# Performance work log

Hardware: AMD Instinct MI355X
Metric: run time of the kernel (lower is better)

Reference implementation:

```python
import jax, jax.numpy as jnp
import numpy as np

ROUTING_ITER = 2
EPS = 1e-8


def squash(s, axis):
    # s * ||s||^2 / (1 + ||s||^2) / ||s||
    sq = jnp.sum(s * s, axis=axis, keepdims=True)
    return s * (sq / (1.0 + sq)) / jnp.sqrt(sq + EPS)


def setup_inputs() -> dict:
    key = jax.random.key(0)
    k1, k2 = jax.random.split(key)
    B, N_in, d_in = 64, 2048, 16
    J, D = 32, 16  # num_capsule, dim_capsule
    x = jax.random.normal(k1, (B, N_in, 1, d_in), dtype=jnp.float32)
    weight = jax.random.normal(k2, (1, N_in, J, D, d_in), dtype=jnp.float32) * 0.05
    return {"x": x, "weight": weight}


def reference(x, weight):
    # x: [B, N_in, 1, d_in]; weight: [1, N_in, J, D, d_in]
    # prediction vectors u[b,i,j,:] = W[i,j] @ x[b,i]
    u = jnp.einsum('ijde,bie->bijd', weight[0], x[:, :, 0, :])  # [B,N_in,J,D]
    B, N_in, J, D = u.shape

    # dynamic routing on stop_gradient(u)
    u_sg = jax.lax.stop_gradient(u)
    b = jnp.zeros((B, N_in, J, 1), dtype=u.dtype)
    for _ in range(ROUTING_ITER):
        c = jax.nn.softmax(b, axis=2)                      # [B,N_in,J,1]
        s = jnp.sum(u_sg * c, axis=1, keepdims=True)       # [B,1,J,D]
        v = squash(s, axis=2)                              # squash over capsule axis (faithful)
        b = b + jnp.sum(u_sg * v, axis=-1, keepdims=True)  # [B,N_in,J,1]

    c = jax.nn.softmax(b, axis=2)
    s = jnp.sum(u * c, axis=1)  # [B,J,D]
    return squash(s, axis=-1)
```

## Files before the change

kernel.cpp:

```cpp
#include <hip/hip_runtime.h>

typedef __attribute__((ext_vector_type(8))) short short8;
typedef __attribute__((ext_vector_type(4))) float f32x4;
typedef __attribute__((ext_vector_type(2))) float f32x2;
typedef __attribute__((ext_vector_type(4))) unsigned int uint4v;
typedef unsigned short u16;
typedef unsigned long long u64;

#define NI 2048

__device__ __forceinline__ unsigned int packbf2(float a, float b){
  unsigned int ua = __float_as_uint(a), ub = __float_as_uint(b);
  unsigned int ra = (ua + 0x7FFFu + ((ua >> 16) & 1u)) >> 16;
  unsigned int rb = (ub + 0x7FFFu + ((ub >> 16) & 1u)) & 0xFFFF0000u;
  return ra | rb;
}
__device__ __forceinline__ float bflo(unsigned int p){ return __uint_as_float(p << 16); }
__device__ __forceinline__ float bfhi(unsigned int p){ return __uint_as_float(p & 0xFFFF0000u); }

__device__ __forceinline__ uint4v cvt8(const f32x4& a, const f32x4& b){
  uint4v p = { packbf2(a.x, a.y), packbf2(a.z, a.w),
               packbf2(b.x, b.y), packbf2(b.z, b.w) };
  return p;
}

__device__ __forceinline__ void gl_lds16(const void* g, void* l){
  __builtin_amdgcn_global_load_lds(
      (const __attribute__((address_space(1))) unsigned int*)g,
      (__attribute__((address_space(3))) unsigned int*)l, 16, 0, 0);
}

union F2U { f32x2 f; u64 u; };

__device__ __forceinline__ void st_u64_coh(float* p, float a, float b){
  F2U v; v.f.x = a; v.f.y = b;
  __hip_atomic_store((u64*)p, v.u, __ATOMIC_RELAXED, __HIP_MEMORY_SCOPE_AGENT);
}
__device__ __forceinline__ f32x2 ld_f2_coh(const float* p){
  F2U v; v.u = __hip_atomic_load((const u64*)p, __ATOMIC_RELAXED, __HIP_MEMORY_SCOPE_AGENT);
  return v.f;
}
__device__ __forceinline__ f32x4 ld_f4_coh(const float* p){
  f32x2 a = ld_f2_coh(p), b = ld_f2_coh(p + 2);
  f32x4 r; r.x = a.x; r.y = a.y; r.z = b.x; r.w = b.y; return r;
}
__device__ __forceinline__ void st_f4_coh(float* p, const f32x4& v){
  st_u64_coh(p, v.x, v.y); st_u64_coh(p + 2, v.z, v.w);
}
__device__ __forceinline__ float ld_f_coh(const float* p){
  return __hip_atomic_load((const float*)p, __ATOMIC_RELAXED, __HIP_MEMORY_SCOPE_AGENT);
}


#define FUSED_SMEM 152576

template<int MODE>
__device__ __forceinline__ void pass_phase(
    const u16* __restrict__ sW, const u16* __restrict__ sX,
    float* __restrict__ sSumA, float* __restrict__ sSumB,
    const float* __restrict__ Sv1, const float* __restrict__ qv1,
    const float* __restrict__ Sv2, const float* __restrict__ qv2,
    float* __restrict__ partials, int blk, int t)
{
  const int w = t >> 6, lane = t & 63;
  const int wtile = w & 1, jhalf = (w >> 1) & 1, bh = w >> 2;
  const int lq = lane >> 4, lb = lane & 15, qs = lq & 1;
  const int bg = bh * 32 + wtile * 16 + lb;
  const short8 zero8 = {0,0,0,0,0,0,0,0};
  const f32x4 zf4 = {0.f,0.f,0.f,0.f};

  f32x4 acc[16];
  #pragma unroll
  for (int tj = 0; tj < 16; ++tj) acc[tj] = zf4;

  unsigned int vpl[16], vph[16];
  if constexpr (MODE >= 1){
    f32x4 qa = ld_f4_coh(qv1 + bg * 16 + lq * 4);
    f32x4 fa;
    fa.x = qa.x / ((1.f + qa.x) * sqrtf(qa.x + 1e-8f));
    fa.y = qa.y / ((1.f + qa.y) * sqrtf(qa.y + 1e-8f));
    fa.z = qa.z / ((1.f + qa.z) * sqrtf(qa.z + 1e-8f));
    fa.w = qa.w / ((1.f + qa.w) * sqrtf(qa.w + 1e-8f));
    f32x4 fb = zf4;
    if constexpr (MODE == 2){
      f32x4 qb = ld_f4_coh(qv2 + bg * 16 + lq * 4);
      fb.x = qb.x / ((1.f + qb.x) * sqrtf(qb.x + 1e-8f));
      fb.y = qb.y / ((1.f + qb.y) * sqrtf(qb.y + 1e-8f));
      fb.z = qb.z / ((1.f + qb.z) * sqrtf(qb.z + 1e-8f));
      fb.w = qb.w / ((1.f + qb.w) * sqrtf(qb.w + 1e-8f));
    }
    #pragma unroll
    for (int tj = 0; tj < 16; ++tj){
      int jd = (jhalf * 16 + tj) * 16 + lq * 4;
      f32x4 sv = ld_f4_coh(Sv1 + bg * 512 + jd);
      f32x4 v;
      v.x = sv.x * fa.x; v.y = sv.y * fa.y; v.z = sv.z * fa.z; v.w = sv.w * fa.w;
      if constexpr (MODE == 2){
        f32x4 s2 = ld_f4_coh(Sv2 + bg * 512 + jd);
        v.x += s2.x * fb.x; v.y += s2.y * fb.y; v.z += s2.z * fb.z; v.w += s2.w * fb.w;
      }
      vpl[tj] = packbf2(v.x, v.y);
      vph[tj] = packbf2(v.z, v.w);
    }
  }

  if constexpr (MODE == 0){
    const int rsel = lq >> 1;
    #pragma unroll
    for (int s = 0; s < 4; ++s){
      const u16* wrow = sW + (size_t)(2 * s + rsel) * 8192;
      const u16* xrow = sX + (size_t)(2 * s + rsel) * 1024;
      short8 bfrag = *(const short8*)(xrow + bg * 16 + qs * 8);
      #pragma unroll
      for (int tj = 0; tj < 16; ++tj){
        int j = jhalf * 16 + tj;
        short8 afrag = *(const short8*)(wrow + j * 256 + lb * 16 + qs * 8);
        acc[tj] = __builtin_amdgcn_mfma_f32_16x16x32_bf16(afrag, bfrag, acc[tj], 0, 0, 0);
      }
    }
  } else {
    for (int s = 0; s < 8; ++s){
      const u16* wrow = sW + (size_t)s * 8192;
      const u16* xrow = sX + (size_t)s * 1024;
      short8 bl8 = *(const short8*)(xrow + bg * 16 + qs * 8);
      short8 bfrag = (lq < 2) ? bl8 : zero8;
      f32x4 ut[16];
      float e[16];
      float ps = 0.f;
      #pragma unroll
      for (int tj = 0; tj < 16; ++tj){
        int j = jhalf * 16 + tj;
        short8 afrag = *(const short8*)(wrow + j * 256 + lb * 16 + qs * 8);
        ut[tj] = __builtin_amdgcn_mfma_f32_16x16x32_bf16(afrag, bfrag, zf4, 0, 0, 0);
        float p = ut[tj].x * bflo(vpl[tj]) + ut[tj].y * bfhi(vpl[tj])
                + ut[tj].z * bflo(vph[tj]) + ut[tj].w * bfhi(vph[tj]);
        p += __shfl_xor(p, 16, 64);
        p += __shfl_xor(p, 32, 64);
        e[tj] = __expf(p);
        ps += e[tj];
      }
      float* sS = (s & 1) ? sSumB : sSumA;
      if (lane < 16) sS[w * 16 + lane] = ps;
      __syncthreads();
      float inv = 1.0f / (ps + sS[(w ^ 2) * 16 + lb]);
      #pragma unroll
      for (int tj = 0; tj < 16; ++tj){
        float c = e[tj] * inv;
        acc[tj].x += c * ut[tj].x;
        acc[tj].y += c * ut[tj].y;
        acc[tj].z += c * ut[tj].z;
        acc[tj].w += c * ut[tj].w;
      }
    }
  }

  float* dst = partials + ((size_t)blk * 8 + (size_t)w) * 4096 + (size_t)lane * 64;
  #pragma unroll
  for (int tj = 0; tj < 16; ++tj) st_f4_coh(dst + tj * 4, acc[tj]);
}

__device__ __forceinline__ void reduce_phase(
    const float* __restrict__ partials, float* __restrict__ S,
    float* __restrict__ qbd, float* __restrict__ qbj,
    float scale, float* __restrict__ sRed, int blk, int t)
{
  const int pr = t & 63;
  const int dg = t >> 6;
  const int o  = blk * 128 + pr * 2;
  const float* src = partials + (size_t)dg * 32 * 32768 + (size_t)o;
  float a0 = 0.f, a1 = 0.f;
  #pragma unroll 8
  for (int p = 0; p < 32; ++p){
    f32x2 v = ld_f2_coh(src + (size_t)p * 32768);
    a0 += v.x; a1 += v.y;
  }
  sRed[t * 2]     = a0;
  sRed[t * 2 + 1] = a1;
  __syncthreads();
  if (t < 64){
    float t0 = 0.f, t1 = 0.f;
    #pragma unroll
    for (int g = 0; g < 8; ++g){
      t0 += sRed[(g * 64 + t) * 2];
      t1 += sRed[(g * 64 + t) * 2 + 1];
    }
    t0 *= scale; t1 *= scale;
    const int oo = blk * 128 + t * 2;
    const int bh = oo >> 14, wd = (oo >> 12) & 3, ln = (oo >> 6) & 63, k = oo & 63;
    const int b = bh * 32 + (wd & 1) * 16 + (ln & 15);
    const int j = (wd >> 1) * 16 + (k >> 2);
    const int d = ((ln >> 4) << 2) + (k & 3);
    st_u64_coh(S + b * 512 + j * 16 + d, t0, t1);
    if (qbd){
      atomicAdd(qbd + b * 16 + d,     t0 * t0);
      atomicAdd(qbd + b * 16 + d + 1, t1 * t1);
    }
    if (qbj){
      atomicAdd(qbj + b * 32 + j, t0 * t0 + t1 * t1);
    }
  }
  __syncthreads();
}

__global__ __launch_bounds__(512, 2)
void caps_fused(const float* __restrict__ X, const float* __restrict__ W,
                unsigned int* __restrict__ gcnt,
                float* __restrict__ qb1, float* __restrict__ qb2,
                float* __restrict__ qb3,
                float* __restrict__ S1, float* __restrict__ S2, float* __restrict__ S3,
                float* __restrict__ partials, float* __restrict__ out)
{
  extern __shared__ __align__(16) char smem[];
  u16* sW = (u16*)smem;
  u16* sX = (u16*)(smem + 131072);
  float* sSumA = (float*)(smem + 147456);
  float* sSumB = sSumA + 128;
  float* sRed  = sSumB + 128;

  const int t = threadIdx.x;
  const int blk = blockIdx.x;
  const size_t i0 = (size_t)blk * 8;

  {
    const float* wsrc = W + i0 * 8192;
    #pragma unroll
    for (int k = 0; k < 16; ++k){
      int idx = k * 4096 + t * 8;
      f32x4 a = *(const f32x4*)(wsrc + idx);
      f32x4 b = *(const f32x4*)(wsrc + idx + 4);
      *(uint4v*)(sW + idx) = cvt8(a, b);
    }
    int r = t >> 6, b = t & 63;
    const float* xs = X + ((size_t)b * NI + i0 + (size_t)r) * 16;
    f32x4 a0 = *(const f32x4*)(xs);
    f32x4 a1 = *(const f32x4*)(xs + 4);
    f32x4 a2 = *(const f32x4*)(xs + 8);
    f32x4 a3 = *(const f32x4*)(xs + 12);
    *(uint4v*)(sX + t * 16)     = cvt8(a0, a1);
    *(uint4v*)(sX + t * 16 + 8) = cvt8(a2, a3);
  }
  __syncthreads();

  unsigned int gen = 0;
  auto gridsync = [&](){
    ++gen;
    __syncthreads();
    if (t == 0){
      __hip_atomic_fetch_add(gcnt, 1u, __ATOMIC_RELAXED, __HIP_MEMORY_SCOPE_AGENT);
      const unsigned int target = gen * 256u;
      while (__hip_atomic_load(gcnt, __ATOMIC_RELAXED, __HIP_MEMORY_SCOPE_AGENT) < target)
        __builtin_amdgcn_s_sleep(8);
    }
    __syncthreads();
  };

  pass_phase<0>(sW, sX, sSumA, sSumB, nullptr, nullptr, nullptr, nullptr, partials, blk, t);
  gridsync();
  reduce_phase(partials, S1, qb1, nullptr, 1.0f / 32.0f, sRed, blk, t);
  gridsync();

  pass_phase<1>(sW, sX, sSumA, sSumB, S1, qb1, nullptr, nullptr, partials, blk, t);
  gridsync();
  reduce_phase(partials, S2, qb2, nullptr, 1.0f, sRed, blk, t);
  gridsync();

  pass_phase<2>(sW, sX, sSumA, sSumB, S1, qb1, S2, qb2, partials, blk, t);
  gridsync();
  reduce_phase(partials, S3, nullptr, qb3, 1.0f, sRed, blk, t);
  gridsync();

  if (blk < 64){
    float s = ld_f_coh(S3 + blk * 512 + t);
    float q = ld_f_coh(qb3 + blk * 32 + (t >> 4));
    out[blk * 512 + t] = s * (q / ((1.f + q) * sqrtf(q + 1e-8f)));
  }
}


__global__ __launch_bounds__(256)
void caps_prep(const float* __restrict__ W, const float* __restrict__ X,
               u16* __restrict__ Wb, u16* __restrict__ Xb)
{
  const int bid = blockIdx.x;
  if (bid < 8192){
    size_t base = (size_t)bid * 2048 + (size_t)threadIdx.x * 8;
    f32x4 a = *(const f32x4*)(W + base);
    f32x4 b = *(const f32x4*)(W + base + 4);
    *(uint4v*)(Wb + base) = cvt8(a, b);
  } else {
    int p = (bid - 8192) * 256 + threadIdx.x;
    int i = p >> 6, b = p & 63;
    const float* src = X + ((size_t)b * NI + i) * 16;
    f32x4 a0 = *(const f32x4*)(src);
    f32x4 a1 = *(const f32x4*)(src + 4);
    f32x4 a2 = *(const f32x4*)(src + 8);
    f32x4 a3 = *(const f32x4*)(src + 12);
    *(uint4v*)(Xb + (size_t)p * 16)     = cvt8(a0, a1);
    *(uint4v*)(Xb + (size_t)p * 16 + 8) = cvt8(a2, a3);
  }
}

template<int MODE>
__global__ __launch_bounds__(256, 2)
void caps_pass_f(const u16* __restrict__ Wb,
                 const u16* __restrict__ Xb,
                 const float* __restrict__ vbuf,
                 float* __restrict__ partials, int CI)
{
  constexpr int WR = (MODE == 0) ? 2 : 1;
  __shared__ __align__(16) u16 sW[2][WR * 8192];
  __shared__ __align__(16) u16 sX[2][WR * 512];
  __shared__ float sSum[4][16];

  const int t     = threadIdx.x;
  const int w     = t >> 6;
  const int lane  = t & 63;
  const int wtile = w & 1;
  const int jhalf = w >> 1;
  const int lq    = lane >> 4;
  const int lb    = lane & 15;
  const int q1    = lq & 1;
  const int bhalf = blockIdx.x & 1;
  const int iblk  = blockIdx.x >> 1;
  const int bloc  = wtile * 16 + lb;
  const int bg    = bhalf * 32 + bloc;
  const size_t i0 = (size_t)iblk * (size_t)CI;

  const short8 zero8 = {0,0,0,0,0,0,0,0};
  const f32x4  zf4   = {0.f,0.f,0.f,0.f};

  f32x4 acc[16];
  #pragma unroll
  for (int tj = 0; tj < 16; ++tj) acc[tj] = zf4;

  unsigned int vpl[16], vph[16];
  if constexpr (MODE == 1){
    #pragma unroll
    for (int tj = 0; tj < 16; ++tj){
      f32x4 v = *(const f32x4*)(&vbuf[bg * 512 + (jhalf * 16 + tj) * 16 + lq * 4]);
      vpl[tj] = packbf2(v.x, v.y);
      vph[tj] = packbf2(v.z, v.w);
    }
  }

  auto stage = [&](int nb, size_t irow){
    #pragma unroll
    for (int rr = 0; rr < WR; ++rr){
      const u16* src = Wb + (irow + rr) * 8192 + (size_t)(w * 4) * 512;
      u16* dst = &sW[nb][rr * 8192 + w * 4 * 512];
      #pragma unroll
      for (int r = 0; r < 4; ++r)
        gl_lds16(src + r * 512 + lane * 8, dst + r * 512);
    }
    if (w >= 4 - WR){
      int rr = w - (4 - WR);
      gl_lds16(Xb + ((irow + rr) * 64 + (size_t)bhalf * 32) * 16 + lane * 8,
               &sX[nb][rr * 512]);
    }
  };

  const int NSTEP = CI / WR;
  stage(0, i0);
  __syncthreads();

  for (int s = 0; s < NSTEP; ++s){
    const int buf = s & 1;
    if (s + 1 < NSTEP) stage(buf ^ 1, i0 + (size_t)(s + 1) * WR);

    if constexpr (MODE == 0){
      const int rsel = lq >> 1;
      short8 bfrag = *(const short8*)(&sX[buf][rsel * 512 + bloc * 16 + q1 * 8]);
      #pragma unroll
      for (int tj = 0; tj < 16; ++tj){
        int j = jhalf * 16 + tj;
        short8 afrag = *(const short8*)(&sW[buf][rsel * 8192 + j * 256 + lb * 16 + q1 * 8]);
        acc[tj] = __builtin_amdgcn_mfma_f32_16x16x32_bf16(afrag, bfrag, acc[tj], 0, 0, 0);
      }
    } else {
      short8 bl8 = *(const short8*)(&sX[buf][bloc * 16 + q1 * 8]);
      short8 bfrag = (lq < 2) ? bl8 : zero8;
      f32x4 ut[16];
      float e[16];
      float ps = 0.f;
      #pragma unroll
      for (int tj = 0; tj < 16; ++tj){
        int j = jhalf * 16 + tj;
        short8 al8 = *(const short8*)(&sW[buf][j * 256 + lb * 16 + q1 * 8]);
        short8 afrag = (lq < 2) ? al8 : zero8;
        ut[tj] = __builtin_amdgcn_mfma_f32_16x16x32_bf16(afrag, bfrag, zf4, 0, 0, 0);
        float p = ut[tj].x * bflo(vpl[tj]) + ut[tj].y * bfhi(vpl[tj])
                + ut[tj].z * bflo(vph[tj]) + ut[tj].w * bfhi(vph[tj]);
        p += __shfl_xor(p, 16, 64);
        p += __shfl_xor(p, 32, 64);
        e[tj] = __expf(p);
        ps += e[tj];
      }
      if (lane < 16) sSum[w][lane] = ps;
      __syncthreads();
      float inv = 1.0f / (ps + sSum[w ^ 2][lb]);
      #pragma unroll
      for (int tj = 0; tj < 16; ++tj){
        float c = e[tj] * inv;
        acc[tj].x += c * ut[tj].x;
        acc[tj].y += c * ut[tj].y;
        acc[tj].z += c * ut[tj].z;
        acc[tj].w += c * ut[tj].w;
      }
    }
    __syncthreads();
  }

  float* dst = partials + ((size_t)blockIdx.x * 4 + (size_t)w) * 4096 + (size_t)lane * 64;
  #pragma unroll
  for (int tj = 0; tj < 16; ++tj) *(f32x4*)(dst + tj * 4) = acc[tj];
}

template<int MODE>
__global__ __launch_bounds__(256)
void caps_pass_legacy(const float* __restrict__ Wg, const float* __restrict__ Xg,
                      const float* __restrict__ vbuf, float* __restrict__ partials, int CI)
{
  __shared__ __align__(16) unsigned short sW[2][8192];
  __shared__ __align__(16) unsigned int   sXd[2][256];
  __shared__ float sLog[(MODE == 1) ? (32 * 33) : 4];
  const int t = threadIdx.x, w = t >> 6, lane = t & 63;
  const int wtile = w & 1, jhalf = w >> 1, lq = lane >> 4, lb = lane & 15, q1 = lq & 1;
  const int bhalf = blockIdx.x & 1, iblk = blockIdx.x >> 1;
  const int bloc = wtile * 16 + lb, bg = bhalf * 32 + bloc;
  const size_t i0 = (size_t)iblk * (size_t)CI;
  const short8 zero8 = {0,0,0,0,0,0,0,0};
  const f32x4 zf4 = {0.f,0.f,0.f,0.f};
  f32x4 acc[16];
  #pragma unroll
  for (int tj = 0; tj < 16; ++tj) acc[tj] = zf4;
  unsigned int vpl[16], vph[16];
  if constexpr (MODE == 1){
    #pragma unroll
    for (int tj = 0; tj < 16; ++tj){
      f32x4 v = *(const f32x4*)(&vbuf[bg * 512 + (jhalf * 16 + tj) * 16 + lq * 4]);
      vpl[tj] = packbf2(v.x, v.y); vph[tj] = packbf2(v.z, v.w);
    }
  }
  {
    const float* wsrc = Wg + i0 * 8192;
    #pragma unroll
    for (int r = 0; r < 4; ++r){
      int c = r * 256 + t;
      f32x4 a = *(const f32x4*)(&wsrc[c * 8]);
      f32x4 b = *(const f32x4*)(&wsrc[c * 8 + 4]);
      *(uint4v*)(&sW[0][c * 8]) = cvt8(a, b);
    }
    int bidx = bhalf * 32 + (t >> 3), e2 = t & 7;
    f32x2 xv = *(const f32x2*)(&Xg[((size_t)bidx * NI + i0) * 16 + e2 * 2]);
    sXd[0][t] = packbf2(xv.x, xv.y);
  }
  __syncthreads();
  for (int s = 0; s < CI; ++s){
    const int buf = s & 1;
    f32x4 wpa[4], wpb[4]; f32x2 xp;
    const bool more = (s + 1 < CI);
    if (more){
      const float* wsrc = Wg + (i0 + (size_t)(s + 1)) * 8192;
      #pragma unroll
      for (int r = 0; r < 4; ++r){
        int c = r * 256 + t;
        wpa[r] = *(const f32x4*)(&wsrc[c * 8]);
        wpb[r] = *(const f32x4*)(&wsrc[c * 8 + 4]);
      }
      int bidx = bhalf * 32 + (t >> 3), e2 = t & 7;
      xp = *(const f32x2*)(&Xg[((size_t)bidx * NI + i0 + s + 1) * 16 + e2 * 2]);
    }
    const unsigned short* xrow = (const unsigned short*)&sXd[buf][0];
    short8 bl8 = *(const short8*)(&xrow[bloc * 16 + q1 * 8]);
    short8 bfrag = (lq < 2) ? bl8 : zero8;
    if constexpr (MODE == 0){
      #pragma unroll
      for (int tj = 0; tj < 16; ++tj){
        int j = jhalf * 16 + tj;
        short8 al8 = *(const short8*)(&sW[buf][j * 256 + lb * 16 + q1 * 8]);
        short8 afrag = (lq < 2) ? al8 : zero8;
        acc[tj] = __builtin_amdgcn_mfma_f32_16x16x32_bf16(afrag, bfrag, acc[tj], 0, 0, 0);
      }
    } else {
      #pragma unroll
      for (int tj = 0; tj < 16; ++tj){
        int j = jhalf * 16 + tj;
        short8 al8 = *(const short8*)(&sW[buf][j * 256 + lb * 16 + q1 * 8]);
        short8 afrag = (lq < 2) ? al8 : zero8;
        f32x4 u = __builtin_amdgcn_mfma_f32_16x16x32_bf16(afrag, bfrag, zf4, 0, 0, 0);
        float p = u.x * bflo(vpl[tj]) + u.y * bfhi(vpl[tj])
                + u.z * bflo(vph[tj]) + u.w * bfhi(vph[tj]);
        p += __shfl_xor(p, 16, 64);
        p += __shfl_xor(p, 32, 64);
        if (lane < 16) sLog[bloc * 33 + j] = p;
      }
      __syncthreads();
      const float* logrow = &sLog[bloc * 33];
      float ssum = 0.f;
      #pragma unroll
      for (int jj = 0; jj < 32; ++jj) ssum += __expf(logrow[jj]);
      float inv = 1.0f / ssum;
      #pragma unroll
      for (int tj = 0; tj < 16; ++tj){
        int j = jhalf * 16 + tj;
        short8 al8 = *(const short8*)(&sW[buf][j * 256 + lb * 16 + q1 * 8]);
        short8 afrag = (lq < 2) ? al8 : zero8;
        f32x4 u = __builtin_amdgcn_mfma_f32_16x16x32_bf16(afrag, bfrag, zf4, 0, 0, 0);
        float c = __expf(logrow[j]) * inv;
        acc[tj].x += c * u.x; acc[tj].y += c * u.y;
        acc[tj].z += c * u.z; acc[tj].w += c * u.w;
      }
    }
    if (more){
      const int nb = buf ^ 1;
      #pragma unroll
      for (int r = 0; r < 4; ++r){
        int c = r * 256 + t;
        *(uint4v*)(&sW[nb][c * 8]) = cvt8(wpa[r], wpb[r]);
      }
      sXd[nb][t] = packbf2(xp.x, xp.y);
    }
    __syncthreads();
  }
  float* dst = partials + ((size_t)blockIdx.x * 4 + (size_t)w) * 4096 + (size_t)lane * 64;
  #pragma unroll
  for (int tj = 0; tj < 16; ++tj) *(f32x4*)(dst + tj * 4) = acc[tj];
}

template<int NBLK>
__global__ __launch_bounds__(128)
void caps_reduce(const float* __restrict__ partials, float* __restrict__ S_buf, float scale)
{
  const int T = blockIdx.x * 128 + threadIdx.x;
  float s0 = 0.f, s1 = 0.f, s2 = 0.f, s3 = 0.f;
  #pragma unroll
  for (int bl = 0; bl < NBLK; bl += 4){
    s0 += partials[(size_t)(bl + 0) * 32768 + T];
    s1 += partials[(size_t)(bl + 1) * 32768 + T];
    s2 += partials[(size_t)(bl + 2) * 32768 + T];
    s3 += partials[(size_t)(bl + 3) * 32768 + T];
  }
  float s = ((s0 + s1) + (s2 + s3)) * scale;
  const int bhalf = T >> 14, w = (T >> 12) & 3, l = (T >> 6) & 63, k = T & 63;
  const int b  = bhalf * 32 + (w & 1) * 16 + (l & 15);
  const int jd = ((w >> 1) * 16 + (k >> 2)) * 16 + ((l >> 4) << 2) + (k & 3);
  S_buf[b * 512 + jd] = s;
}

__global__ __launch_bounds__(256)
void caps_squash_j(const float* __restrict__ S, const float* __restrict__ vprev,
                   float* __restrict__ vout)
{
  const int b = blockIdx.x, t = threadIdx.x;
  __shared__ float sq[16];
  if (t < 16) sq[t] = 0.f;
  __syncthreads();
  float s0 = S[b * 512 + t], s1 = S[b * 512 + 256 + t];
  atomicAdd(&sq[t & 15], s0 * s0 + s1 * s1);
  __syncthreads();
  float q = sq[t & 15];
  float f = q / ((1.f + q) * sqrtf(q + 1e-8f));
  float v0 = s0 * f, v1 = s1 * f;
  if (vprev){ v0 += vprev[b * 512 + t]; v1 += vprev[b * 512 + 256 + t]; }
  vout[b * 512 + t] = v0;
  vout[b * 512 + 256 + t] = v1;
}

__global__ __launch_bounds__(256)
void caps_squash_d(const float* __restrict__ S, float* __restrict__ out)
{
  const int b = blockIdx.x, t = threadIdx.x;
  __shared__ float sq[32];
  if (t < 32) sq[t] = 0.f;
  __syncthreads();
  float s0 = S[b * 512 + t], s1 = S[b * 512 + 256 + t];
  atomicAdd(&sq[t >> 4], s0 * s0);
  atomicAdd(&sq[(t + 256) >> 4], s1 * s1);
  __syncthreads();
  float q0 = sq[t >> 4], q1 = sq[(t + 256) >> 4];
  out[b * 512 + t]       = s0 * q0 / ((1.f + q0) * sqrtf(q0 + 1e-8f));
  out[b * 512 + 256 + t] = s1 * q1 / ((1.f + q1) * sqrtf(q1 + 1e-8f));
}

extern "C" void kernel_launch(void* const* d_in, const int* in_sizes, int n_in,
                              void* d_out, int out_size, void* d_ws, size_t ws_size,
                              hipStream_t stream)
{
  const float* X = (const float*)d_in[0];
  const float* W = (const float*)d_in[1];
  float* wsf = (float*)d_ws;

  const size_t OF_Q1   = 64;
  const size_t OF_Q2   = OF_Q1 + 1024;
  const size_t OF_Q3   = OF_Q2 + 1024;
  const size_t OF_S1   = OF_Q3 + 2048;
  const size_t OF_S2   = OF_S1 + 32768;
  const size_t OF_S3   = OF_S2 + 32768;
  const size_t OF_PART = OF_S3 + 32768;
  const size_t FUSED_FLOATS = OF_PART + (size_t)256 * 32768;

  static int fused_ok = -1;
  if (fused_ok < 0){
    fused_ok = 0;
    hipFuncSetAttribute(reinterpret_cast<const void*>(caps_fused),
                        hipFuncAttributeMaxDynamicSharedMemorySize, FUSED_SMEM);
    int dev = 0, ncu = 0, nb = 0;
    hipGetDevice(&dev);
    hipDeviceGetAttribute(&ncu, hipDeviceAttributeMultiprocessorCount, dev);
    hipError_t e = hipOccupancyMaxActiveBlocksPerMultiprocessor(
        &nb, caps_fused, 512, (size_t)FUSED_SMEM);
    if (e == hipSuccess && nb >= 1 && ncu >= 256) fused_ok = 1;
  }

  if (fused_ok == 1 && ws_size >= FUSED_FLOATS * 4){
    hipMemsetAsync(d_ws, 0, (64 + 1024 + 1024 + 2048) * 4, stream);
    caps_fused<<<dim3(256), dim3(512), FUSED_SMEM, stream>>>(
        X, W, (unsigned int*)wsf,
        wsf + OF_Q1, wsf + OF_Q2, wsf + OF_Q3,
        wsf + OF_S1, wsf + OF_S2, wsf + OF_S3, wsf + OF_PART, (float*)d_out);
    return;
  }

  const size_t FP = (size_t)256 * 32768;
  const size_t WB_ELE = (size_t)NI * 8192, XB_ELE = (size_t)NI * 64 * 16;
  const size_t need_full = (FP + 3 * 32768) * 4 + (WB_ELE + XB_ELE) * 2;

  if (ws_size >= need_full){
    float* partials = wsf;
    float* sbuf = wsf + FP;
    float* v1   = sbuf + 32768;
    float* v12  = v1 + 32768;
    u16* Wb = (u16*)(v12 + 32768);
    u16* Xb = Wb + WB_ELE;

    caps_prep<<<dim3(8704), dim3(256), 0, stream>>>(W, X, Wb, Xb);

    caps_pass_f<0><<<dim3(512), dim3(256), 0, stream>>>(Wb, Xb, nullptr, partials, 8);
    caps_reduce<256><<<dim3(256), dim3(128), 0, stream>>>(partials, sbuf, 1.0f / 32.0f);
    caps_squash_j<<<dim3(64), dim3(256), 0, stream>>>(sbuf, nullptr, v1);

    caps_pass_f<1><<<dim3(512), dim3(256), 0, stream>>>(Wb, Xb, v1, partials, 8);
    caps_reduce<256><<<dim3(256), dim3(128), 0, stream>>>(partials, sbuf, 1.0f);
    caps_squash_j<<<dim3(64), dim3(256), 0, stream>>>(sbuf, v1, v12);

    caps_pass_f<1><<<dim3(512), dim3(256), 0, stream>>>(Wb, Xb, v12, partials, 8);
    caps_reduce<256><<<dim3(256), dim3(128), 0, stream>>>(partials, sbuf, 1.0f);
    caps_squash_d<<<dim3(64), dim3(256), 0, stream>>>(sbuf, (float*)d_out);
  } else {
    int NBI = 256;
    auto need = [](int nb){ return ((size_t)nb * 32768 + 3 * 32768) * 4; };
    if (ws_size < need(256)){
      if      (ws_size >= need(64)) NBI = 64;
      else if (ws_size >= need(16)) NBI = 16;
      else                          NBI = 4;
    }
    const int CI = NI / NBI;
    float* partials = wsf;
    float* sbuf = wsf + (size_t)NBI * 32768;
    float* v1   = sbuf + 32768;
    float* v12  = v1 + 32768;
    auto reduce = [&](float scale){
      if      (NBI == 256) caps_reduce<256><<<dim3(256), dim3(128), 0, stream>>>(partials, sbuf, scale);
      else if (NBI ==  64) caps_reduce< 64><<<dim3(256), dim3(128), 0, stream>>>(partials, sbuf, scale);
      else if (NBI ==  16) caps_reduce< 16><<<dim3(256), dim3(128), 0, stream>>>(partials, sbuf, scale);
      else                 caps_reduce<  4><<<dim3(256), dim3(128), 0, stream>>>(partials, sbuf, scale);
    };
    caps_pass_legacy<0><<<dim3(2 * NBI), dim3(256), 0, stream>>>(W, X, nullptr, partials, CI);
    reduce(1.0f / 32.0f);
    caps_squash_j<<<dim3(64), dim3(256), 0, stream>>>(sbuf, nullptr, v1);
    caps_pass_legacy<1><<<dim3(2 * NBI), dim3(256), 0, stream>>>(W, X, v1, partials, CI);
    reduce(1.0f);
    caps_squash_j<<<dim3(64), dim3(256), 0, stream>>>(sbuf, v1, v12);
    caps_pass_legacy<1><<<dim3(2 * NBI), dim3(256), 0, stream>>>(W, X, v12, partials, CI);
    reduce(1.0f);
    caps_squash_d<<<dim3(64), dim3(256), 0, stream>>>(sbuf, (float*)d_out);
  }
}
```

Before: 233.7 us.

## Use hierarchical grid barrier, batched 16-byte coherent loads, and wider reduction

```diff
diff --git a/kernel.cpp b/kernel.cpp
--- a/kernel.cpp
+++ b/kernel.cpp
@@ -30,29 +30,33 @@
       (__attribute__((address_space(3))) unsigned int*)l, 16, 0, 0);
 }
 
-union F2U { f32x2 f; u64 u; };
-
-__device__ __forceinline__ void st_u64_coh(float* p, float a, float b){
-  F2U v; v.f.x = a; v.f.y = b;
-  __hip_atomic_store((u64*)p, v.u, __ATOMIC_RELAXED, __HIP_MEMORY_SCOPE_AGENT);
-}
-__device__ __forceinline__ f32x2 ld_f2_coh(const float* p){
-  F2U v; v.u = __hip_atomic_load((const u64*)p, __ATOMIC_RELAXED, __HIP_MEMORY_SCOPE_AGENT);
-  return v.f;
-}
-__device__ __forceinline__ f32x4 ld_f4_coh(const float* p){
-  f32x2 a = ld_f2_coh(p), b = ld_f2_coh(p + 2);
-  f32x4 r; r.x = a.x; r.y = a.y; r.z = b.x; r.w = b.y; return r;
-}
-__device__ __forceinline__ void st_f4_coh(float* p, const f32x4& v){
-  st_u64_coh(p, v.x, v.y); st_u64_coh(p + 2, v.z, v.w);
+__device__ __forceinline__ void st16_coh(float* p, f32x4 v){
+  asm volatile("global_store_dwordx4 %0, %1, off sc1" :: "v"(p), "v"(v) : "memory");
+}
+__device__ __forceinline__ f32x4 ld16_coh(const float* p){
+  f32x4 r;
+  asm volatile("global_load_dwordx4 %0, %1, off sc1" : "=v"(r) : "v"(p) : "memory");
+  return r;
+}
+__device__ __forceinline__ void vm_drain(){
+  asm volatile("s_waitcnt vmcnt(0)" ::: "memory");
+  __builtin_amdgcn_sched_barrier(0);
 }
 __device__ __forceinline__ float ld_f_coh(const float* p){
-  return __hip_atomic_load((const float*)p, __ATOMIC_RELAXED, __HIP_MEMORY_SCOPE_AGENT);
-}
-
-
-#define FUSED_SMEM 152576
+  return __hip_atomic_load(p, __ATOMIC_RELAXED, __HIP_MEMORY_SCOPE_AGENT);
+}
+
+__device__ __forceinline__ f32x4 squash4(const f32x4& q){
+  f32x4 f;
+  f.x = q.x / ((1.f + q.x) * sqrtf(q.x + 1e-8f));
+  f.y = q.y / ((1.f + q.y) * sqrtf(q.y + 1e-8f));
+  f.z = q.z / ((1.f + q.z) * sqrtf(q.z + 1e-8f));
+  f.w = q.w / ((1.f + q.w) * sqrtf(q.w + 1e-8f));
+  return f;
+}
+
+
+#define FUSED_SMEM 156672
 
 template<int MODE>
 __device__ __forceinline__ void pass_phase(
@@ -75,32 +79,53 @@
 
   unsigned int vpl[16], vph[16];
   if constexpr (MODE >= 1){
-    f32x4 qa = ld_f4_coh(qv1 + bg * 16 + lq * 4);
-    f32x4 fa;
-    fa.x = qa.x / ((1.f + qa.x) * sqrtf(qa.x + 1e-8f));
-    fa.y = qa.y / ((1.f + qa.y) * sqrtf(qa.y + 1e-8f));
-    fa.z = qa.z / ((1.f + qa.z) * sqrtf(qa.z + 1e-8f));
-    fa.w = qa.w / ((1.f + qa.w) * sqrtf(qa.w + 1e-8f));
+    f32x4 qa = ld16_coh(qv1 + bg * 16 + lq * 4);
+    f32x4 qb;
+    if constexpr (MODE == 2) qb = ld16_coh(qv2 + bg * 16 + lq * 4);
+    vm_drain();
+    f32x4 fa = squash4(qa);
     f32x4 fb = zf4;
+    if constexpr (MODE == 2) fb = squash4(qb);
+
+    f32x4 vv[16];
+    #pragma unroll
+    for (int g = 0; g < 2; ++g){
+      f32x4 sv[8];
+      #pragma unroll
+      for (int m = 0; m < 8; ++m){
+        int tj = g * 8 + m;
+        sv[m] = ld16_coh(Sv1 + bg * 512 + (jhalf * 16 + tj) * 16 + lq * 4);
+      }
+      vm_drain();
+      #pragma unroll
+      for (int m = 0; m < 8; ++m){
+        int tj = g * 8 + m;
+        vv[tj].x = sv[m].x * fa.x; vv[tj].y = sv[m].y * fa.y;
+        vv[tj].z = sv[m].z * fa.z; vv[tj].w = sv[m].w * fa.w;
+      }
+    }
     if constexpr (MODE == 2){
-      f32x4 qb = ld_f4_coh(qv2 + bg * 16 + lq * 4);
-      fb.x = qb.x / ((1.f + qb.x) * sqrtf(qb.x + 1e-8f));
-      fb.y = qb.y / ((1.f + qb.y) * sqrtf(qb.y + 1e-8f));
-      fb.z = qb.z / ((1.f + qb.z) * sqrtf(qb.z + 1e-8f));
-      fb.w = qb.w / ((1.f + qb.w) * sqrtf(qb.w + 1e-8f));
+      #pragma unroll
+      for (int g = 0; g < 2; ++g){
+        f32x4 sv[8];
+        #pragma unroll
+        for (int m = 0; m < 8; ++m){
+          int tj = g * 8 + m;
+          sv[m] = ld16_coh(Sv2 + bg * 512 + (jhalf * 16 + tj) * 16 + lq * 4);
+        }
+        vm_drain();
+        #pragma unroll
+        for (int m = 0; m < 8; ++m){
+          int tj = g * 8 + m;
+          vv[tj].x += sv[m].x * fb.x; vv[tj].y += sv[m].y * fb.y;
+          vv[tj].z += sv[m].z * fb.z; vv[tj].w += sv[m].w * fb.w;
+        }
+      }
     }
     #pragma unroll
     for (int tj = 0; tj < 16; ++tj){
-      int jd = (jhalf * 16 + tj) * 16 + lq * 4;
-      f32x4 sv = ld_f4_coh(Sv1 + bg * 512 + jd);
-      f32x4 v;
-      v.x = sv.x * fa.x; v.y = sv.y * fa.y; v.z = sv.z * fa.z; v.w = sv.w * fa.w;
-      if constexpr (MODE == 2){
-        f32x4 s2 = ld_f4_coh(Sv2 + bg * 512 + jd);
-        v.x += s2.x * fb.x; v.y += s2.y * fb.y; v.z += s2.z * fb.z; v.w += s2.w * fb.w;
-      }
-      vpl[tj] = packbf2(v.x, v.y);
-      vph[tj] = packbf2(v.z, v.w);
+      vpl[tj] = packbf2(vv[tj].x, vv[tj].y);
+      vph[tj] = packbf2(vv[tj].z, vv[tj].w);
     }
   }
 
@@ -156,48 +181,47 @@
 
   float* dst = partials + ((size_t)blk * 8 + (size_t)w) * 4096 + (size_t)lane * 64;
   #pragma unroll
-  for (int tj = 0; tj < 16; ++tj) st_f4_coh(dst + tj * 4, acc[tj]);
+  for (int tj = 0; tj < 16; ++tj) st16_coh(dst + tj * 4, acc[tj]);
 }
 
 __device__ __forceinline__ void reduce_phase(
     const float* __restrict__ partials, float* __restrict__ S,
     float* __restrict__ qbd, float* __restrict__ qbj,
-    float scale, float* __restrict__ sRed, int blk, int t)
-{
-  const int pr = t & 63;
-  const int dg = t >> 6;
-  const int o  = blk * 128 + pr * 2;
-  const float* src = partials + (size_t)dg * 32 * 32768 + (size_t)o;
-  float a0 = 0.f, a1 = 0.f;
-  #pragma unroll 8
-  for (int p = 0; p < 32; ++p){
-    f32x2 v = ld_f2_coh(src + (size_t)p * 32768);
-    a0 += v.x; a1 += v.y;
-  }
-  sRed[t * 2]     = a0;
-  sRed[t * 2 + 1] = a1;
-  __syncthreads();
-  if (t < 64){
-    float t0 = 0.f, t1 = 0.f;
-    #pragma unroll
-    for (int g = 0; g < 8; ++g){
-      t0 += sRed[(g * 64 + t) * 2];
-      t1 += sRed[(g * 64 + t) * 2 + 1];
-    }
-    t0 *= scale; t1 *= scale;
-    const int oo = blk * 128 + t * 2;
-    const int bh = oo >> 14, wd = (oo >> 12) & 3, ln = (oo >> 6) & 63, k = oo & 63;
+    float scale, f32x4* __restrict__ sRed4, int blk, int t)
+{
+  const int qd = t & 31;
+  const int dg = t >> 5;
+  const float* src = partials + (size_t)dg * 16 * 32768 + (size_t)blk * 128 + qd * 4;
+  f32x4 ld[16];
+  #pragma unroll
+  for (int p = 0; p < 16; ++p) ld[p] = ld16_coh(src + (size_t)p * 32768);
+  vm_drain();
+  f32x4 a = ld[0];
+  #pragma unroll
+  for (int p = 1; p < 16; ++p){ a.x += ld[p].x; a.y += ld[p].y; a.z += ld[p].z; a.w += ld[p].w; }
+  sRed4[t] = a;
+  __syncthreads();
+  if (t < 32){
+    f32x4 s = sRed4[t];
+    #pragma unroll
+    for (int g = 1; g < 16; ++g){
+      f32x4 r = sRed4[g * 32 + t];
+      s.x += r.x; s.y += r.y; s.z += r.z; s.w += r.w;
+    }
+    s.x *= scale; s.y *= scale; s.z *= scale; s.w *= scale;
+    const int oo = blk * 128 + t * 4;
+    const int k = oo & 63, ln = (oo >> 6) & 63, wd = (oo >> 12) & 3, bh = oo >> 14;
     const int b = bh * 32 + (wd & 1) * 16 + (ln & 15);
     const int j = (wd >> 1) * 16 + (k >> 2);
-    const int d = ((ln >> 4) << 2) + (k & 3);
-    st_u64_coh(S + b * 512 + j * 16 + d, t0, t1);
+    const int d0 = (ln >> 4) << 2;
+    st16_coh(S + b * 512 + j * 16 + d0, s);
     if (qbd){
-      atomicAdd(qbd + b * 16 + d,     t0 * t0);
-      atomicAdd(qbd + b * 16 + d + 1, t1 * t1);
-    }
-    if (qbj){
-      atomicAdd(qbj + b * 32 + j, t0 * t0 + t1 * t1);
-    }
+      atomicAdd(qbd + b * 16 + d0 + 0, s.x * s.x);
+      atomicAdd(qbd + b * 16 + d0 + 1, s.y * s.y);
+      atomicAdd(qbd + b * 16 + d0 + 2, s.z * s.z);
+      atomicAdd(qbd + b * 16 + d0 + 3, s.w * s.w);
+    }
+    if (qbj) atomicAdd(qbj + b * 32 + j, s.x * s.x + s.y * s.y + s.z * s.z + s.w * s.w);
   }
   __syncthreads();
 }
@@ -214,8 +238,8 @@
   u16* sW = (u16*)smem;
   u16* sX = (u16*)(smem + 131072);
   float* sSumA = (float*)(smem + 147456);
-  float* sSumB = sSumA + 128;
-  float* sRed  = sSumB + 128;
+  float* sSumB = (float*)(smem + 147968);
+  f32x4* sRed4 = (f32x4*)(smem + 148480);
 
   const int t = threadIdx.x;
   const int blk = blockIdx.x;
@@ -242,32 +266,47 @@
   __syncthreads();
 
   unsigned int gen = 0;
-  auto gridsync = [&](){
+  auto gridsync = [&](bool wait){
     ++gen;
+    asm volatile("s_waitcnt vmcnt(0)" ::: "memory");
     __syncthreads();
     if (t == 0){
-      __hip_atomic_fetch_add(gcnt, 1u, __ATOMIC_RELAXED, __HIP_MEMORY_SCOPE_AGENT);
-      const unsigned int target = gen * 256u;
-      while (__hip_atomic_load(gcnt, __ATOMIC_RELAXED, __HIP_MEMORY_SCOPE_AGENT) < target)
-        __builtin_amdgcn_s_sleep(8);
+      __hip_atomic_fetch_add(gcnt + (blk & 7) * 4, 1u,
+                             __ATOMIC_RELAXED, __HIP_MEMORY_SCOPE_AGENT);
+      if (blk == 0){
+        #pragma unroll 1
+        for (int g = 0; g < 8; ++g){
+          while (__hip_atomic_load(gcnt + g * 4, __ATOMIC_RELAXED,
+                                   __HIP_MEMORY_SCOPE_AGENT) < gen * 32u)
+            __builtin_amdgcn_s_sleep(2);
+        }
+        #pragma unroll
+        for (int g = 0; g < 8; ++g)
+          __hip_atomic_store(gcnt + 64 + g * 64, gen,
+                             __ATOMIC_RELAXED, __HIP_MEMORY_SCOPE_AGENT);
+      } else if (wait){
+        while (__hip_atomic_load(gcnt + 64 + (blk & 7) * 64, __ATOMIC_RELAXED,
+                                 __HIP_MEMORY_SCOPE_AGENT) < gen)
+          __builtin_amdgcn_s_sleep(2);
+      }
     }
     __syncthreads();
   };
 
   pass_phase<0>(sW, sX, sSumA, sSumB, nullptr, nullptr, nullptr, nullptr, partials, blk, t);
-  gridsync();
-  reduce_phase(partials, S1, qb1, nullptr, 1.0f / 32.0f, sRed, blk, t);
-  gridsync();
+  gridsync(true);
+  reduce_phase(partials, S1, qb1, nullptr, 1.0f / 32.0f, sRed4, blk, t);
+  gridsync(true);
 
   pass_phase<1>(sW, sX, sSumA, sSumB, S1, qb1, nullptr, nullptr, partials, blk, t);
-  gridsync();
-  reduce_phase(partials, S2, qb2, nullptr, 1.0f, sRed, blk, t);
-  gridsync();
+  gridsync(true);
+  reduce_phase(partials, S2, qb2, nullptr, 1.0f, sRed4, blk, t);
+  gridsync(true);
 
   pass_phase<2>(sW, sX, sSumA, sSumB, S1, qb1, S2, qb2, partials, blk, t);
-  gridsync();
-  reduce_phase(partials, S3, nullptr, qb3, 1.0f, sRed, blk, t);
-  gridsync();
+  gridsync(true);
+  reduce_phase(partials, S3, nullptr, qb3, 1.0f, sRed4, blk, t);
+  gridsync(blk < 64);
 
   if (blk < 64){
     float s = ld_f_coh(S3 + blk * 512 + t);
@@ -590,7 +629,7 @@
   const float* W = (const float*)d_in[1];
   float* wsf = (float*)d_ws;
 
-  const size_t OF_Q1   = 64;
+  const size_t OF_Q1   = 1024;
   const size_t OF_Q2   = OF_Q1 + 1024;
   const size_t OF_Q3   = OF_Q2 + 1024;
   const size_t OF_S1   = OF_Q3 + 2048;
@@ -613,7 +652,7 @@
   }
 
   if (fused_ok == 1 && ws_size >= FUSED_FLOATS * 4){
-    hipMemsetAsync(d_ws, 0, (64 + 1024 + 1024 + 2048) * 4, stream);
+    hipMemsetAsync(d_ws, 0, (1024 + 1024 + 1024 + 2048) * 4, stream);
     caps_fused<<<dim3(256), dim3(512), FUSED_SMEM, stream>>>(
         X, W, (unsigned int*)wsf,
         wsf + OF_Q1, wsf + OF_Q2, wsf + OF_Q3,
```

Measured after the change: 232.2 us. About the same (-0.6%).
